# Kernel tuning notes

Measured on AMD Instinct MI355X. Metric: run time of the kernel, lower is better.

## Reference

```python
import jax, jax.numpy as jnp
import numpy as np

N = 100000   # nodes
E = 800000   # edges
IN, HID, H, OUT = 128, 32, 4, 16
NEG_SLOPE = 0.2


def _gatv2_layer(x, src, dst, Ws, bs, Wd, bd, attn, heads, dim):
    # fc_src / fc_dst projections -> [N, H, D]
    hs = (x @ Ws + bs).reshape(-1, heads, dim)
    hd = (x @ Wd + bd).reshape(-1, heads, dim)
    # per-edge GATv2 score: leaky_relu(h_src[u] + h_dst[v]) . attn
    e = jax.nn.leaky_relu(hs[src] + hd[dst], negative_slope=NEG_SLOPE)  # [E,H,D]
    score = jnp.einsum('ehd,hd->eh', e, attn)                           # [E,H]
    # edge softmax grouped by destination node (stable)
    m = jax.ops.segment_max(score, dst, num_segments=N)
    m = jax.lax.stop_gradient(jnp.where(jnp.isfinite(m), m, 0.0))
    ex = jnp.exp(score - m[dst])
    denom = jax.ops.segment_sum(ex, dst, num_segments=N)
    alpha = ex / denom[dst]                                             # [E,H]
    # scatter-sum aggregation of alpha * h_src back to destination nodes
    return jax.ops.segment_sum(alpha[:, :, None] * hs[src], dst, num_segments=N)


def setup_inputs() -> dict:
    key = jax.random.key(0)
    ks = jax.random.split(key, 12)
    feats = jax.random.normal(ks[0], (N, IN), dtype=jnp.float32)
    edge_index = jax.random.randint(ks[1], (2, E), 0, N)
    s1 = 1.0 / np.sqrt(IN)
    s2 = 1.0 / np.sqrt(HID * H)
    return {
        'features': feats,
        'edge_index': edge_index,
        'W1s': jax.random.normal(ks[2], (IN, H * HID), dtype=jnp.float32) * s1,
        'b1s': jnp.zeros((H * HID,), dtype=jnp.float32),
        'W1d': jax.random.normal(ks[3], (IN, H * HID), dtype=jnp.float32) * s1,
        'b1d': jnp.zeros((H * HID,), dtype=jnp.float32),
        'attn1': jax.random.normal(ks[4], (H, HID), dtype=jnp.float32) * (1.0 / np.sqrt(HID)),
        'W2s': jax.random.normal(ks[5], (H * HID, OUT), dtype=jnp.float32) * s2,
        'b2s': jnp.zeros((OUT,), dtype=jnp.float32),
        'W2d': jax.random.normal(ks[6], (H * HID, OUT), dtype=jnp.float32) * s2,
        'b2d': jnp.zeros((OUT,), dtype=jnp.float32),
        'attn2': jax.random.normal(ks[7], (1, OUT), dtype=jnp.float32) * (1.0 / np.sqrt(OUT)),
    }


def reference(features, edge_index, W1s, b1s, W1d, b1d, attn1, W2s, b2s, W2d, b2d, attn2):
    src, dst = edge_index[0], edge_index[1]
    h = _gatv2_layer(features, src, dst, W1s, b1s, W1d, b1d, attn1, H, HID)
    h = jax.nn.elu(h.reshape(N, H * HID))                 # flatten(1) + elu
    out = _gatv2_layer(h, src, dst, W2s, b2s, W2d, b2d, attn2, 1, OUT)
    return out.reshape(N, OUT)                            # squeeze(1)
```

## Files before the change

kernel.cpp:

```cpp
#include <hip/hip_runtime.h>
#include <hip/hip_bf16.h>


#define NEG_SLOPE 0.2f

typedef _Float16 f16;
typedef _Float16 f16x2 __attribute__((ext_vector_type(2)));
typedef _Float16 f16x4 __attribute__((ext_vector_type(4)));
typedef _Float16 f16x8 __attribute__((ext_vector_type(8)));
typedef float f32x4 __attribute__((ext_vector_type(4)));

__global__ __launch_bounds__(256) void k_hist(const int* __restrict__ dst, int* __restrict__ cnt,
                                              int* __restrict__ rank, int e) {
    int i = blockIdx.x * 256 + threadIdx.x;
    if (i < e) rank[i] = atomicAdd(&cnt[dst[i]], 1);
}

__global__ __launch_bounds__(256) void k_scan1(const int* __restrict__ cnt, int* __restrict__ offs,
                                               int* __restrict__ bsum, int n) {
    __shared__ int sh[256];
    int t = threadIdx.x;
    int base = blockIdx.x * 1024 + t * 4;
    int v[4]; int s = 0;
    #pragma unroll
    for (int j = 0; j < 4; ++j) { v[j] = (base + j < n) ? cnt[base + j] : 0; s += v[j]; }
    sh[t] = s; __syncthreads();
    for (int o = 1; o < 256; o <<= 1) {
        int x = (t >= o) ? sh[t - o] : 0;
        __syncthreads();
        sh[t] += x;
        __syncthreads();
    }
    int excl = sh[t] - s;
    if (t == 255) bsum[blockIdx.x] = sh[255];
    int run = excl;
    #pragma unroll
    for (int j = 0; j < 4; ++j) {
        if (base + j < n) { offs[base + j] = run; run += v[j]; }
    }
}

__global__ __launch_bounds__(256) void k_scan2(int* __restrict__ bsum, int nb) {
    __shared__ int sh[256];
    int t = threadIdx.x;
    int val = (t < nb) ? bsum[t] : 0;
    sh[t] = val; __syncthreads();
    for (int o = 1; o < 256; o <<= 1) {
        int x = (t >= o) ? sh[t - o] : 0;
        __syncthreads();
        sh[t] += x;
        __syncthreads();
    }
    if (t < nb) bsum[t] = sh[t] - val;
}

__global__ __launch_bounds__(256) void k_scan3(int* __restrict__ offs, const int* __restrict__ bsum,
                                               int n, int e) {
    int i = blockIdx.x * 256 + threadIdx.x;
    if (i < n) offs[i] += bsum[i >> 10];
    if (i == 0) offs[n] = e;
}

__global__ __launch_bounds__(256) void k_scatter(const int* __restrict__ src, const int* __restrict__ dst,
                                                 const int* __restrict__ offs, const int* __restrict__ rank,
                                                 int* __restrict__ ssrc, int e) {
    int i = blockIdx.x * 256 + threadIdx.x;
    if (i < e) {
        int pos = offs[dst[i]] + rank[i];
        ssrc[pos] = src[i];
    }
}

__global__ __launch_bounds__(128) void k_pre(const float* __restrict__ W1s, const float* __restrict__ W1d,
                                             const float* __restrict__ W2s, const float* __restrict__ W2d,
                                             const float* __restrict__ attn1, const float* __restrict__ attn2,
                                             f16* __restrict__ Bh, f16* __restrict__ Bh2,
                                             f16* __restrict__ attnh, int* __restrict__ cnt, int n) {
    int b = blockIdx.x, k = threadIdx.x;
    if (b < 256) {
        float v = (b < 128) ? W1s[k * 128 + b] : W1d[k * 128 + (b - 128)];
        int idx = (((b >> 4) * 16 + (k >> 3)) * 16 + (b & 15)) * 8 + (k & 7);
        Bh[idx] = (f16)v;
    } else if (b < 288) {
        int c = b - 256;
        float v = (c < 16) ? W2s[k * 16 + c] : W2d[k * 16 + (c - 16)];
        Bh2[c * 128 + k] = (f16)v;
    } else if (b == 288) {
        attnh[k] = (f16)attn1[k];
        if (k < 16) attnh[128 + k] = (f16)attn2[k];
    } else {
        int i = ((b - 289) * 128 + k) * 4;
        if (i < n) {
            int m = n - i;
            if (m > 4) m = 4;
            for (int j = 0; j < m; ++j) cnt[i + j] = 0;
        }
    }
}

__global__ __launch_bounds__(256) void k_proj1_mfma(
    const float* __restrict__ x, const f16* __restrict__ Bh,
    const float* __restrict__ bs, const float* __restrict__ bd,
    f16* __restrict__ hs, f16* __restrict__ hd, int n)
{
    __shared__ __align__(16) char lds[2 * 32 * 256];
    char* alds = lds;
    char* elds = lds + 8192;
    int t = threadIdx.x;
    int row0 = blockIdx.x * 32;

    {
        const float4* x4 = reinterpret_cast<const float4*>(x + (size_t)row0 * 128);
        int rows_here = n - row0; if (rows_here > 32) rows_here = 32;
        int max4 = rows_here * 32;
        #pragma unroll
        for (int i = 0; i < 4; ++i) {
            int idx = t + i * 256;
            float4 v = (idx < max4) ? x4[idx] : make_float4(0.f, 0.f, 0.f, 0.f);
            int row = idx >> 5, k = (idx & 31) * 4;
            int off = row * 256 + ((((k >> 3) ^ (row & 7)) & 15) << 4) + (k & 7) * 2;
            f16x4 h; h[0] = (f16)v.x; h[1] = (f16)v.y; h[2] = (f16)v.z; h[3] = (f16)v.w;
            *reinterpret_cast<f16x4*>(alds + off) = h;
        }
    }
    __syncthreads();

    int w = t >> 6, lane = t & 63;
    int n0w = w * 32;
    int lr = lane & 15;
    int kgrp = lane >> 4;
    int nc0 = kgrp * 4;

    for (int half = 0; half < 2; ++half) {
        f32x4 acc[2][2] = {};
        #pragma unroll
        for (int ks = 0; ks < 4; ++ks) {
            int k = ks * 32 + kgrp * 8;
            f16x8 b[2], a[2];
            #pragma unroll
            for (int nf = 0; nf < 2; ++nf) {
                int cg = half * 8 + w * 2 + nf;
                const f16* Bf = Bh + (size_t)cg * 2048 + ((ks * 4 + kgrp) * 16 + lr) * 8;
                b[nf] = *reinterpret_cast<const f16x8*>(Bf);
            }
            #pragma unroll
            for (int mf = 0; mf < 2; ++mf) {
                int row = mf * 16 + lr;
                int off = row * 256 + ((((k >> 3) ^ (row & 7)) & 15) << 4);
                a[mf] = *reinterpret_cast<const f16x8*>(alds + off);
            }
            #pragma unroll
            for (int mf = 0; mf < 2; ++mf)
                #pragma unroll
                for (int nf = 0; nf < 2; ++nf)
                    acc[mf][nf] = __builtin_amdgcn_mfma_f32_16x16x32_f16(b[nf], a[mf], acc[mf][nf], 0, 0, 0);
        }

        const float* bias = half ? bd : bs;
        #pragma unroll
        for (int mf = 0; mf < 2; ++mf) {
            int row = mf * 16 + lr;
            #pragma unroll
            for (int nf = 0; nf < 2; ++nf) {
                int col = n0w + nf * 16 + nc0;
                float4 bv = *reinterpret_cast<const float4*>(bias + col);
                f16x4 o;
                o[0] = (f16)(acc[mf][nf][0] + bv.x);
                o[1] = (f16)(acc[mf][nf][1] + bv.y);
                o[2] = (f16)(acc[mf][nf][2] + bv.z);
                o[3] = (f16)(acc[mf][nf][3] + bv.w);
                int off = row * 256 + ((col * 2) ^ ((row & 7) << 4));
                *reinterpret_cast<f16x4*>(elds + off) = o;
            }
        }
        __syncthreads();

        f16* outp = half ? hd : hs;
        #pragma unroll
        for (int j = 0; j < 2; ++j) {
            int c = t + j * 256;
            int row = c >> 4;
            int colb = (c & 15) * 16;
            f16x8 vv = *reinterpret_cast<const f16x8*>(elds + row * 256 + (colb ^ ((row & 7) << 4)));
            int grow = row0 + row;
            if (grow < n)
                *reinterpret_cast<f16x8*>(outp + (size_t)grow * 128 + colb / 2) = vv;
        }
        __syncthreads();
    }
}

__global__ __launch_bounds__(256) void k_edge1(
    const f16* __restrict__ hs, const f16* __restrict__ hd,
    const f16* __restrict__ attnh,
    const int* __restrict__ offs, const int* __restrict__ ssrc,
    f16* __restrict__ out, int n)
{
    int wid = (blockIdx.x * 256 + threadIdx.x) >> 6;
    int lane = threadIdx.x & 63;
    int sub = lane >> 4;
    int q = lane & 15;
    int v = wid * 4 + sub;
    if (v >= n) return;
    int lbase = sub << 4;

    f16x8 hd8 = *reinterpret_cast<const f16x8*>(hd + (size_t)v * 128 + 8 * q);
    f16x8 a8  = *reinterpret_cast<const f16x8*>(attnh + 8 * q);
    const f16x2* a2 = reinterpret_cast<const f16x2*>(&a8);

    int beg = offs[v], end = offs[v + 1];
    float s = 0.f;
    float acc[8] = {};

    for (int chunk = beg; chunk < end; chunk += 16) {
        int cnt = end - chunk; if (cnt > 16) cnt = 16;
        int idxv = (q < cnt) ? ssrc[chunk + q] : 0;

        int u0 = __builtin_amdgcn_ds_bpermute((lbase + 0) << 2, idxv);
        f16x8 hu0 = {};
        if (0 < cnt) hu0 = *reinterpret_cast<const f16x8*>(hs + (size_t)u0 * 128 + 8 * q);
        int u1 = __builtin_amdgcn_ds_bpermute((lbase + 1) << 2, idxv);
        f16x8 hu1 = {};
        if (1 < cnt) hu1 = *reinterpret_cast<const f16x8*>(hs + (size_t)u1 * 128 + 8 * q);

        for (int e = 0; e < cnt; ++e) {
            int u2 = __builtin_amdgcn_ds_bpermute((lbase + ((e + 2) & 15)) << 2, idxv);
            f16x8 hu2 = {};
            if (e + 2 < cnt) hu2 = *reinterpret_cast<const f16x8*>(hs + (size_t)u2 * 128 + 8 * q);

            f16x8 t  = hu0 + hd8;
            f16x8 at = __builtin_elementwise_abs(t);
            const f16x2* t2  = reinterpret_cast<const f16x2*>(&t);
            const f16x2* at2 = reinterpret_cast<const f16x2*>(&at);
            float p = 0.f, r = 0.f;
            #pragma unroll
            for (int j = 0; j < 4; ++j) {
                p = __builtin_amdgcn_fdot2(t2[j],  a2[j], p, false);
                r = __builtin_amdgcn_fdot2(at2[j], a2[j], r, false);
            }
            float sc = 0.6f * p + 0.4f * r;
            sc += __shfl_xor(sc, 1);
            sc += __shfl_xor(sc, 2);
            float w = __expf(sc);
            s += w;
            #pragma unroll
            for (int j = 0; j < 8; ++j) acc[j] = fmaf(w, (float)hu0[j], acc[j]);
            hu0 = hu1; hu1 = hu2;
        }
    }

    float inv = s > 0.f ? 1.f / s : 0.f;
    f16x8 o;
    #pragma unroll
    for (int j = 0; j < 8; ++j) o[j] = (f16)(acc[j] * inv);
    *reinterpret_cast<f16x8*>(out + (size_t)v * 128 + 8 * q) = o;
}

__global__ __launch_bounds__(256) void k_proj2_mfma(
    const f16* __restrict__ h_in, const f16* __restrict__ Bh2,
    const float* __restrict__ bs, const float* __restrict__ bd,
    f16* __restrict__ hs, f16* __restrict__ hd, int n)
{
    __shared__ __align__(16) char lds[128 * 256];
    int t = threadIdx.x;
    int row0 = blockIdx.x * 128;

    {
        int row = t >> 1, half = t & 1;
        bool valid = (row0 + row) < n;
        const f16x8* xr = reinterpret_cast<const f16x8*>(h_in + (size_t)(row0 + row) * 128);
        #pragma unroll
        for (int i = 0; i < 8; ++i) {
            int q = half * 8 + i;
            f16x8 vv = {};
            if (valid) vv = xr[q];
            f16x8 ov;
            #pragma unroll
            for (int j = 0; j < 8; ++j) {
                float f = (float)vv[j];
                f = f > 0.f ? f : __expf(f) - 1.f;
                ov[j] = (f16)f;
            }
            int off = row * 256 + (((q ^ (row & 7)) & 15) << 4);
            *reinterpret_cast<f16x8*>(lds + off) = ov;
        }
    }
    __syncthreads();

    int w = t >> 6, lane = t & 63;
    int lr = lane & 15;
    int kgrp = lane >> 4;

    f32x4 acc[2][2] = {};
    #pragma unroll
    for (int ks = 0; ks < 4; ++ks) {
        int k = ks * 32 + kgrp * 8;
        f16x8 b[2], a[2];
        #pragma unroll
        for (int nf = 0; nf < 2; ++nf)
            b[nf] = *reinterpret_cast<const f16x8*>(Bh2 + (nf * 16 + lr) * 128 + k);
        #pragma unroll
        for (int mf = 0; mf < 2; ++mf) {
            int row = w * 32 + mf * 16 + lr;
            int off = row * 256 + ((((k >> 3) ^ (row & 7)) & 15) << 4);
            a[mf] = *reinterpret_cast<const f16x8*>(lds + off);
        }
        #pragma unroll
        for (int mf = 0; mf < 2; ++mf)
            #pragma unroll
            for (int nf = 0; nf < 2; ++nf)
                acc[mf][nf] = __builtin_amdgcn_mfma_f32_16x16x32_f16(b[nf], a[mf], acc[mf][nf], 0, 0, 0);
    }

    int nc0 = kgrp * 4;
    #pragma unroll
    for (int mf = 0; mf < 2; ++mf) {
        int grow = row0 + w * 32 + mf * 16 + lr;
        if (grow < n) {
            #pragma unroll
            for (int nf = 0; nf < 2; ++nf) {
                const float* bp = (nf == 0) ? (bs + nc0) : (bd + nc0);
                f16* outp = (nf == 0) ? hs : hd;
                float4 bv = *reinterpret_cast<const float4*>(bp);
                f16x4 o;
                o[0] = (f16)(acc[mf][nf][0] + bv.x);
                o[1] = (f16)(acc[mf][nf][1] + bv.y);
                o[2] = (f16)(acc[mf][nf][2] + bv.z);
                o[3] = (f16)(acc[mf][nf][3] + bv.w);
                *reinterpret_cast<f16x4*>(outp + (size_t)grow * 16 + nc0) = o;
            }
        }
    }
}

__global__ __launch_bounds__(256) void k_edge2(
    const f16* __restrict__ hs, const f16* __restrict__ hd,
    const f16* __restrict__ attnh,
    const int* __restrict__ offs, const int* __restrict__ ssrc,
    float* __restrict__ out, int n)
{
    int wid = (blockIdx.x * 256 + threadIdx.x) >> 6;
    int lane = threadIdx.x & 63;
    int sub = lane >> 4;
    int i16 = lane & 15;
    int g = i16 >> 2;
    int slot = i16 & 3;
    int v = wid * 4 + sub;
    if (v >= n) return;
    int lbase = sub << 4;

    f16x4 hd4 = *reinterpret_cast<const f16x4*>(hd + (size_t)v * 16 + 4 * slot);
    f16x4 a4  = *reinterpret_cast<const f16x4*>(attnh + 4 * slot);
    const f16x2* a2 = reinterpret_cast<const f16x2*>(&a4);

    int beg = offs[v], end = offs[v + 1];
    float s = 0.f;
    float acc[4] = {};

    for (int chunk = beg; chunk < end; chunk += 16) {
        int cnt = end - chunk; if (cnt > 16) cnt = 16;
        int idxv = (i16 < cnt) ? ssrc[chunk + i16] : 0;
        int nIter = (cnt + 3) >> 2;

        int u0 = __builtin_amdgcn_ds_bpermute((lbase + g) << 2, idxv);
        f16x4 hu0 = {};
        if (g < cnt) hu0 = *reinterpret_cast<const f16x4*>(hs + (size_t)u0 * 16 + 4 * slot);
        int u1 = __builtin_amdgcn_ds_bpermute((lbase + ((g + 4) & 15)) << 2, idxv);
        f16x4 hu1 = {};
        if (g + 4 < cnt) hu1 = *reinterpret_cast<const f16x4*>(hs + (size_t)u1 * 16 + 4 * slot);

        for (int it = 0; it < nIter; ++it) {
            int e2 = g + 4 * it + 8;
            int u2 = __builtin_amdgcn_ds_bpermute((lbase + (e2 & 15)) << 2, idxv);
            f16x4 hu2 = {};
            if (e2 < cnt) hu2 = *reinterpret_cast<const f16x4*>(hs + (size_t)u2 * 16 + 4 * slot);

            bool valid = (g + 4 * it) < cnt;
            f16x4 t  = hu0 + hd4;
            f16x4 at = __builtin_elementwise_abs(t);
            const f16x2* t2  = reinterpret_cast<const f16x2*>(&t);
            const f16x2* at2 = reinterpret_cast<const f16x2*>(&at);
            float p = 0.f, r = 0.f;
            #pragma unroll
            for (int j = 0; j < 2; ++j) {
                p = __builtin_amdgcn_fdot2(t2[j],  a2[j], p, false);
                r = __builtin_amdgcn_fdot2(at2[j], a2[j], r, false);
            }
            float sc = 0.6f * p + 0.4f * r;
            sc += __shfl_xor(sc, 1);
            sc += __shfl_xor(sc, 2);
            float w = valid ? __expf(sc) : 0.f;
            s += w;
            #pragma unroll
            for (int j = 0; j < 4; ++j) acc[j] = fmaf(w, (float)hu0[j], acc[j]);
            hu0 = hu1; hu1 = hu2;
        }
    }

    #pragma unroll
    for (int st = 0; st < 2; ++st) {
        int off = 4 << st;
        s += __shfl_xor(s, off);
        #pragma unroll
        for (int j = 0; j < 4; ++j) acc[j] += __shfl_xor(acc[j], off);
    }

    if (g == 0) {
        float inv = s > 0.f ? 1.f / s : 0.f;
        float4 o = make_float4(acc[0] * inv, acc[1] * inv, acc[2] * inv, acc[3] * inv);
        *reinterpret_cast<float4*>(out + (size_t)v * 16 + 4 * slot) = o;
    }
}

extern "C" void kernel_launch(void* const* d_in, const int* in_sizes, int n_in,
                              void* d_out, int out_size, void* d_ws, size_t ws_size,
                              hipStream_t stream) {
    const float* x     = (const float*)d_in[0];
    const int*   ei    = (const int*)d_in[1];
    const float* W1s   = (const float*)d_in[2];
    const float* b1s   = (const float*)d_in[3];
    const float* W1d   = (const float*)d_in[4];
    const float* b1d   = (const float*)d_in[5];
    const float* attn1 = (const float*)d_in[6];
    const float* W2s   = (const float*)d_in[7];
    const float* b2s   = (const float*)d_in[8];
    const float* W2d   = (const float*)d_in[9];
    const float* b2d   = (const float*)d_in[10];
    const float* attn2 = (const float*)d_in[11];

    int n = in_sizes[0] / 128;
    int e = in_sizes[1] / 2;
    const int* src = ei;
    const int* dst = ei + e;

    char* base = (char*)d_ws;
    size_t off = 0;
    auto alloc = [&](size_t bytes) {
        char* p = base + off;
        off = (off + bytes + 255) & ~255ULL;
        return p;
    };
    int* offs   = (int*)alloc((size_t)(n + 1) * 4);
    int* cnt    = (int*)alloc((size_t)n * 4);
    int* rank   = (int*)alloc((size_t)e * 4);
    int* ssrc   = (int*)alloc((size_t)e * 4);
    int* bsum   = (int*)alloc(256 * 4);
    f16* Bh     = (f16*)alloc(256 * 128 * 2);
    f16* Bh2    = (f16*)alloc(32 * 128 * 2);
    f16* attnh  = (f16*)alloc(144 * 2);
    f16* hs1    = (f16*)alloc((size_t)n * 128 * 2);
    f16* hd1    = (f16*)alloc((size_t)n * 128 * 2);
    f16* out1   = (f16*)alloc((size_t)n * 128 * 2);
    f16* hs2    = (f16*)alloc((size_t)n * 16 * 2);
    f16* hd2    = (f16*)alloc((size_t)n * 16 * 2);
    (void)ws_size;

    int nb = (n + 1023) / 1024;
    int zeroB = (n + 511) / 512;

    k_pre<<<289 + zeroB, 128, 0, stream>>>(W1s, W1d, W2s, W2d, attn1, attn2,
                                           Bh, Bh2, attnh, cnt, n);
    k_hist<<<(e + 255) / 256, 256, 0, stream>>>(dst, cnt, rank, e);
    k_scan1<<<nb, 256, 0, stream>>>(cnt, offs, bsum, n);
    k_scan2<<<1, 256, 0, stream>>>(bsum, nb);
    k_scan3<<<(n + 255) / 256, 256, 0, stream>>>(offs, bsum, n, e);
    k_scatter<<<(e + 255) / 256, 256, 0, stream>>>(src, dst, offs, rank, ssrc, e);

    k_proj1_mfma<<<(n + 31) / 32, 256, 0, stream>>>(x, Bh, b1s, b1d, hs1, hd1, n);
    k_edge1<<<(n + 15) / 16, 256, 0, stream>>>(hs1, hd1, attnh, offs, ssrc, out1, n);
    k_proj2_mfma<<<(n + 127) / 128, 256, 0, stream>>>(out1, Bh2, b2s, b2d, hs2, hd2, n);
    k_edge2<<<(n + 15) / 16, 256, 0, stream>>>(hs2, hd2, attnh + 128, offs, ssrc, (float*)d_out, n);
}
```

Baseline: 159.0 us.

## Replace CSR build with fixed-capacity per-node buckets and overflow list

Removes the histogram, three-pass scan and scatter kernels used to build CSR by destination. Edges are appended directly into per-node buckets of fixed capacity 64 with one atomic per edge, and any extra edges go to a global overflow list. The edge kernels then read neighbors from the bucket and linearly scan the overflow list for high-degree nodes. This saves four kernel launches and two passes over the edges, at the cost of a larger sparse bucket array with scattered writes and a slow fallback if any node exceeds the cap.

```diff
diff --git a/kernel.cpp b/kernel.cpp
--- a/kernel.cpp
+++ b/kernel.cpp
@@ -3,6 +3,7 @@
 
 
 #define NEG_SLOPE 0.2f
+#define CAP 64
 
 typedef _Float16 f16;
 typedef _Float16 f16x2 __attribute__((ext_vector_type(2)));
@@ -10,64 +11,19 @@
 typedef _Float16 f16x8 __attribute__((ext_vector_type(8)));
 typedef float f32x4 __attribute__((ext_vector_type(4)));
 
-__global__ __launch_bounds__(256) void k_hist(const int* __restrict__ dst, int* __restrict__ cnt,
-                                              int* __restrict__ rank, int e) {
-    int i = blockIdx.x * 256 + threadIdx.x;
-    if (i < e) rank[i] = atomicAdd(&cnt[dst[i]], 1);
-}
-
-__global__ __launch_bounds__(256) void k_scan1(const int* __restrict__ cnt, int* __restrict__ offs,
-                                               int* __restrict__ bsum, int n) {
-    __shared__ int sh[256];
-    int t = threadIdx.x;
-    int base = blockIdx.x * 1024 + t * 4;
-    int v[4]; int s = 0;
-    #pragma unroll
-    for (int j = 0; j < 4; ++j) { v[j] = (base + j < n) ? cnt[base + j] : 0; s += v[j]; }
-    sh[t] = s; __syncthreads();
-    for (int o = 1; o < 256; o <<= 1) {
-        int x = (t >= o) ? sh[t - o] : 0;
-        __syncthreads();
-        sh[t] += x;
-        __syncthreads();
-    }
-    int excl = sh[t] - s;
-    if (t == 255) bsum[blockIdx.x] = sh[255];
-    int run = excl;
-    #pragma unroll
-    for (int j = 0; j < 4; ++j) {
-        if (base + j < n) { offs[base + j] = run; run += v[j]; }
-    }
-}
-
-__global__ __launch_bounds__(256) void k_scan2(int* __restrict__ bsum, int nb) {
-    __shared__ int sh[256];
-    int t = threadIdx.x;
-    int val = (t < nb) ? bsum[t] : 0;
-    sh[t] = val; __syncthreads();
-    for (int o = 1; o < 256; o <<= 1) {
-        int x = (t >= o) ? sh[t - o] : 0;
-        __syncthreads();
-        sh[t] += x;
-        __syncthreads();
-    }
-    if (t < nb) bsum[t] = sh[t] - val;
-}
-
-__global__ __launch_bounds__(256) void k_scan3(int* __restrict__ offs, const int* __restrict__ bsum,
-                                               int n, int e) {
-    int i = blockIdx.x * 256 + threadIdx.x;
-    if (i < n) offs[i] += bsum[i >> 10];
-    if (i == 0) offs[n] = e;
-}
-
-__global__ __launch_bounds__(256) void k_scatter(const int* __restrict__ src, const int* __restrict__ dst,
-                                                 const int* __restrict__ offs, const int* __restrict__ rank,
-                                                 int* __restrict__ ssrc, int e) {
+__global__ __launch_bounds__(256) void k_build(const int* __restrict__ src, const int* __restrict__ dst,
+                                               int* __restrict__ cnt, int* __restrict__ bucket,
+                                               int* __restrict__ ovf, int* __restrict__ ovf_cnt, int e) {
     int i = blockIdx.x * 256 + threadIdx.x;
     if (i < e) {
-        int pos = offs[dst[i]] + rank[i];
-        ssrc[pos] = src[i];
+        int d = dst[i];
+        int r = atomicAdd(&cnt[d], 1);
+        if (r < CAP) {
+            bucket[(size_t)d * CAP + r] = src[i];
+        } else {
+            int o = atomicAdd(ovf_cnt, 1);
+            ovf[2 * o] = d; ovf[2 * o + 1] = src[i];
+        }
     }
 }
 
@@ -75,7 +31,8 @@
                                              const float* __restrict__ W2s, const float* __restrict__ W2d,
                                              const float* __restrict__ attn1, const float* __restrict__ attn2,
                                              f16* __restrict__ Bh, f16* __restrict__ Bh2,
-                                             f16* __restrict__ attnh, int* __restrict__ cnt, int n) {
+                                             f16* __restrict__ attnh, int* __restrict__ cnt,
+                                             int* __restrict__ ovf_cnt, int n) {
     int b = blockIdx.x, k = threadIdx.x;
     if (b < 256) {
         float v = (b < 128) ? W1s[k * 128 + b] : W1d[k * 128 + (b - 128)];
@@ -88,6 +45,7 @@
     } else if (b == 288) {
         attnh[k] = (f16)attn1[k];
         if (k < 16) attnh[128 + k] = (f16)attn2[k];
+        if (k == 0) ovf_cnt[0] = 0;
     } else {
         int i = ((b - 289) * 128 + k) * 4;
         if (i < n) {
@@ -193,7 +151,8 @@
 __global__ __launch_bounds__(256) void k_edge1(
     const f16* __restrict__ hs, const f16* __restrict__ hd,
     const f16* __restrict__ attnh,
-    const int* __restrict__ offs, const int* __restrict__ ssrc,
+    const int* __restrict__ cnt, const int* __restrict__ bucket,
+    const int* __restrict__ ovf, const int* __restrict__ ovf_cnt,
     f16* __restrict__ out, int n)
 {
     int wid = (blockIdx.x * 256 + threadIdx.x) >> 6;
@@ -208,25 +167,27 @@
     f16x8 a8  = *reinterpret_cast<const f16x8*>(attnh + 8 * q);
     const f16x2* a2 = reinterpret_cast<const f16x2*>(&a8);
 
-    int beg = offs[v], end = offs[v + 1];
+    int deg = cnt[v];
+    int end = deg < CAP ? deg : CAP;
+    const int* bk = bucket + (size_t)v * CAP;
     float s = 0.f;
     float acc[8] = {};
 
-    for (int chunk = beg; chunk < end; chunk += 16) {
-        int cnt = end - chunk; if (cnt > 16) cnt = 16;
-        int idxv = (q < cnt) ? ssrc[chunk + q] : 0;
+    for (int chunk = 0; chunk < end; chunk += 16) {
+        int c = end - chunk; if (c > 16) c = 16;
+        int idxv = (q < c) ? bk[chunk + q] : 0;
 
         int u0 = __builtin_amdgcn_ds_bpermute((lbase + 0) << 2, idxv);
         f16x8 hu0 = {};
-        if (0 < cnt) hu0 = *reinterpret_cast<const f16x8*>(hs + (size_t)u0 * 128 + 8 * q);
+        if (0 < c) hu0 = *reinterpret_cast<const f16x8*>(hs + (size_t)u0 * 128 + 8 * q);
         int u1 = __builtin_amdgcn_ds_bpermute((lbase + 1) << 2, idxv);
         f16x8 hu1 = {};
-        if (1 < cnt) hu1 = *reinterpret_cast<const f16x8*>(hs + (size_t)u1 * 128 + 8 * q);
-
-        for (int e = 0; e < cnt; ++e) {
+        if (1 < c) hu1 = *reinterpret_cast<const f16x8*>(hs + (size_t)u1 * 128 + 8 * q);
+
+        for (int e = 0; e < c; ++e) {
             int u2 = __builtin_amdgcn_ds_bpermute((lbase + ((e + 2) & 15)) << 2, idxv);
             f16x8 hu2 = {};
-            if (e + 2 < cnt) hu2 = *reinterpret_cast<const f16x8*>(hs + (size_t)u2 * 128 + 8 * q);
+            if (e + 2 < c) hu2 = *reinterpret_cast<const f16x8*>(hs + (size_t)u2 * 128 + 8 * q);
 
             f16x8 t  = hu0 + hd8;
             f16x8 at = __builtin_elementwise_abs(t);
@@ -246,6 +207,33 @@
             #pragma unroll
             for (int j = 0; j < 8; ++j) acc[j] = fmaf(w, (float)hu0[j], acc[j]);
             hu0 = hu1; hu1 = hu2;
+        }
+    }
+
+    if (deg > CAP) {
+        int m = *ovf_cnt;
+        for (int j = 0; j < m; ++j) {
+            if (ovf[2 * j] == v) {
+                int u = ovf[2 * j + 1];
+                f16x8 hu = *reinterpret_cast<const f16x8*>(hs + (size_t)u * 128 + 8 * q);
+                f16x8 t  = hu + hd8;
+                f16x8 at = __builtin_elementwise_abs(t);
+                const f16x2* t2  = reinterpret_cast<const f16x2*>(&t);
+                const f16x2* at2 = reinterpret_cast<const f16x2*>(&at);
+                float p = 0.f, r = 0.f;
+                #pragma unroll
+                for (int jj = 0; jj < 4; ++jj) {
+                    p = __builtin_amdgcn_fdot2(t2[jj],  a2[jj], p, false);
+                    r = __builtin_amdgcn_fdot2(at2[jj], a2[jj], r, false);
+                }
+                float sc = 0.6f * p + 0.4f * r;
+                sc += __shfl_xor(sc, 1);
+                sc += __shfl_xor(sc, 2);
+                float w = __expf(sc);
+                s += w;
+                #pragma unroll
+                for (int jj = 0; jj < 8; ++jj) acc[jj] = fmaf(w, (float)hu[jj], acc[jj]);
+            }
         }
     }
 
@@ -336,7 +324,8 @@
 __global__ __launch_bounds__(256) void k_edge2(
     const f16* __restrict__ hs, const f16* __restrict__ hd,
     const f16* __restrict__ attnh,
-    const int* __restrict__ offs, const int* __restrict__ ssrc,
+    const int* __restrict__ cnt, const int* __restrict__ bucket,
+    const int* __restrict__ ovf, const int* __restrict__ ovf_cnt,
     float* __restrict__ out, int n)
 {
     int wid = (blockIdx.x * 256 + threadIdx.x) >> 6;
@@ -353,29 +342,31 @@
     f16x4 a4  = *reinterpret_cast<const f16x4*>(attnh + 4 * slot);
     const f16x2* a2 = reinterpret_cast<const f16x2*>(&a4);
 
-    int beg = offs[v], end = offs[v + 1];
+    int deg = cnt[v];
+    int end = deg < CAP ? deg : CAP;
+    const int* bk = bucket + (size_t)v * CAP;
     float s = 0.f;
     float acc[4] = {};
 
-    for (int chunk = beg; chunk < end; chunk += 16) {
-        int cnt = end - chunk; if (cnt > 16) cnt = 16;
-        int idxv = (i16 < cnt) ? ssrc[chunk + i16] : 0;
-        int nIter = (cnt + 3) >> 2;
+    for (int chunk = 0; chunk < end; chunk += 16) {
+        int c = end - chunk; if (c > 16) c = 16;
+        int idxv = (i16 < c) ? bk[chunk + i16] : 0;
+        int nIter = (c + 3) >> 2;
 
         int u0 = __builtin_amdgcn_ds_bpermute((lbase + g) << 2, idxv);
         f16x4 hu0 = {};
-        if (g < cnt) hu0 = *reinterpret_cast<const f16x4*>(hs + (size_t)u0 * 16 + 4 * slot);
+        if (g < c) hu0 = *reinterpret_cast<const f16x4*>(hs + (size_t)u0 * 16 + 4 * slot);
         int u1 = __builtin_amdgcn_ds_bpermute((lbase + ((g + 4) & 15)) << 2, idxv);
         f16x4 hu1 = {};
-        if (g + 4 < cnt) hu1 = *reinterpret_cast<const f16x4*>(hs + (size_t)u1 * 16 + 4 * slot);
+        if (g + 4 < c) hu1 = *reinterpret_cast<const f16x4*>(hs + (size_t)u1 * 16 + 4 * slot);
 
         for (int it = 0; it < nIter; ++it) {
             int e2 = g + 4 * it + 8;
             int u2 = __builtin_amdgcn_ds_bpermute((lbase + (e2 & 15)) << 2, idxv);
             f16x4 hu2 = {};
-            if (e2 < cnt) hu2 = *reinterpret_cast<const f16x4*>(hs + (size_t)u2 * 16 + 4 * slot);
-
-            bool valid = (g + 4 * it) < cnt;
+            if (e2 < c) hu2 = *reinterpret_cast<const f16x4*>(hs + (size_t)u2 * 16 + 4 * slot);
+
+            bool valid = (g + 4 * it) < c;
             f16x4 t  = hu0 + hd4;
             f16x4 at = __builtin_elementwise_abs(t);
             const f16x2* t2  = reinterpret_cast<const f16x2*>(&t);
@@ -394,6 +385,34 @@
             #pragma unroll
             for (int j = 0; j < 4; ++j) acc[j] = fmaf(w, (float)hu0[j], acc[j]);
             hu0 = hu1; hu1 = hu2;
+        }
+    }
+
+    if (deg > CAP) {
+        int m = *ovf_cnt;
+        for (int j = 0; j < m; ++j) {
+            int dv = ovf[2 * j];
+            if (dv == v) {
+                int u = ovf[2 * j + 1];
+                f16x4 hu = *reinterpret_cast<const f16x4*>(hs + (size_t)u * 16 + 4 * slot);
+                f16x4 t  = hu + hd4;
+                f16x4 at = __builtin_elementwise_abs(t);
+                const f16x2* t2  = reinterpret_cast<const f16x2*>(&t);
+                const f16x2* at2 = reinterpret_cast<const f16x2*>(&at);
+                float p = 0.f, r = 0.f;
+                #pragma unroll
+                for (int jj = 0; jj < 2; ++jj) {
+                    p = __builtin_amdgcn_fdot2(t2[jj],  a2[jj], p, false);
+                    r = __builtin_amdgcn_fdot2(at2[jj], a2[jj], r, false);
+                }
+                float sc = 0.6f * p + 0.4f * r;
+                sc += __shfl_xor(sc, 1);
+                sc += __shfl_xor(sc, 2);
+                float w = (g == 0) ? __expf(sc) : 0.f;
+                s += w;
+                #pragma unroll
+                for (int jj = 0; jj < 4; ++jj) acc[jj] = fmaf(w, (float)hu[jj], acc[jj]);
+            }
         }
     }
 
@@ -440,34 +459,27 @@
         off = (off + bytes + 255) & ~255ULL;
         return p;
     };
-    int* offs   = (int*)alloc((size_t)(n + 1) * 4);
-    int* cnt    = (int*)alloc((size_t)n * 4);
-    int* rank   = (int*)alloc((size_t)e * 4);
-    int* ssrc   = (int*)alloc((size_t)e * 4);
-    int* bsum   = (int*)alloc(256 * 4);
-    f16* Bh     = (f16*)alloc(256 * 128 * 2);
-    f16* Bh2    = (f16*)alloc(32 * 128 * 2);
-    f16* attnh  = (f16*)alloc(144 * 2);
-    f16* hs1    = (f16*)alloc((size_t)n * 128 * 2);
-    f16* hd1    = (f16*)alloc((size_t)n * 128 * 2);
-    f16* out1   = (f16*)alloc((size_t)n * 128 * 2);
-    f16* hs2    = (f16*)alloc((size_t)n * 16 * 2);
-    f16* hd2    = (f16*)alloc((size_t)n * 16 * 2);
+    int* cnt     = (int*)alloc((size_t)n * 4);
+    int* bucket  = (int*)alloc((size_t)n * CAP * 4);
+    int* ovf     = (int*)alloc((size_t)e * 8);
+    int* ovf_cnt = (int*)alloc(256);
+    f16* Bh      = (f16*)alloc(256 * 128 * 2);
+    f16* Bh2     = (f16*)alloc(32 * 128 * 2);
+    f16* attnh   = (f16*)alloc(144 * 2);
+    f16* hs1     = (f16*)alloc((size_t)n * 128 * 2);
+    f16* hd1     = (f16*)alloc((size_t)n * 128 * 2);
+    f16* out1    = (f16*)alloc((size_t)n * 128 * 2);
+    f16* hs2     = (f16*)alloc((size_t)n * 16 * 2);
+    f16* hd2     = (f16*)alloc((size_t)n * 16 * 2);
     (void)ws_size;
 
-    int nb = (n + 1023) / 1024;
     int zeroB = (n + 511) / 512;
 
     k_pre<<<289 + zeroB, 128, 0, stream>>>(W1s, W1d, W2s, W2d, attn1, attn2,
-                                           Bh, Bh2, attnh, cnt, n);
-    k_hist<<<(e + 255) / 256, 256, 0, stream>>>(dst, cnt, rank, e);
-    k_scan1<<<nb, 256, 0, stream>>>(cnt, offs, bsum, n);
-    k_scan2<<<1, 256, 0, stream>>>(bsum, nb);
-    k_scan3<<<(n + 255) / 256, 256, 0, stream>>>(offs, bsum, n, e);
-    k_scatter<<<(e + 255) / 256, 256, 0, stream>>>(src, dst, offs, rank, ssrc, e);
-
+                                           Bh, Bh2, attnh, cnt, ovf_cnt, n);
+    k_build<<<(e + 255) / 256, 256, 0, stream>>>(src, dst, cnt, bucket, ovf, ovf_cnt, e);
     k_proj1_mfma<<<(n + 31) / 32, 256, 0, stream>>>(x, Bh, b1s, b1d, hs1, hd1, n);
-    k_edge1<<<(n + 15) / 16, 256, 0, stream>>>(hs1, hd1, attnh, offs, ssrc, out1, n);
+    k_edge1<<<(n + 15) / 16, 256, 0, stream>>>(hs1, hd1, attnh, cnt, bucket, ovf, ovf_cnt, out1, n);
     k_proj2_mfma<<<(n + 127) / 128, 256, 0, stream>>>(out1, Bh2, b2s, b2d, hs2, hd2, n);
-    k_edge2<<<(n + 15) / 16, 256, 0, stream>>>(hs2, hd2, attnh + 128, offs, ssrc, (float*)d_out, n);
-}
+    k_edge2<<<(n + 15) / 16, 256, 0, stream>>>(hs2, hd2, attnh + 128, cnt, bucket, ovf, ovf_cnt, (float*)d_out, n);
+}
```

Result: faster. 152.8 us (-3.9%).
